# Kernel optimization log

Measured on AMD Instinct MI355X. Metric: run time of the kernel, lower is better.

Reference implementation:

```python
import jax, jax.numpy as jnp
import numpy as np

WS = 7        # window_size
NH = 12       # num_heads
HD = 32       # head_dim
SCALE = HD ** -0.5


def _rel_pos_index(ws: int) -> np.ndarray:
    # Static [N, N] index into the (2ws-1)^2 relative position bias table.
    coords = np.stack(np.meshgrid(np.arange(ws), np.arange(ws), indexing='ij'))
    coords = coords.reshape(2, -1)                       # [2, N]
    rel = coords[:, :, None] - coords[:, None, :]        # [2, N, N]
    rel = rel.transpose(1, 2, 0).copy()                  # [N, N, 2]
    rel[:, :, 0] += ws - 1
    rel[:, :, 1] += ws - 1
    rel[:, :, 0] *= 2 * ws - 1
    return rel.sum(-1)                                   # [N, N]

_REL_IDX = jnp.asarray(_rel_pos_index(WS))


def setup_inputs() -> dict:
    key = jax.random.key(0)
    ks = jax.random.split(key, 7)
    BW, N, C = 2048, WS * WS, 384
    nW = 64
    return {
        'x': jax.random.normal(ks[0], (BW, N, C), jnp.float32),
        'mask': jax.random.normal(ks[1], (nW, N, N), jnp.float32),
        'qkv_w': jax.random.normal(ks[2], (3 * C, C), jnp.float32) * 0.02,
        'qkv_b': jax.random.normal(ks[3], (3 * C,), jnp.float32) * 0.02,
        'proj_w': jax.random.normal(ks[4], (C, C), jnp.float32) * 0.02,
        'proj_b': jax.random.normal(ks[5], (C,), jnp.float32) * 0.02,
        'bias_table': jax.random.normal(ks[6], ((2 * WS - 1) ** 2, NH), jnp.float32) * 0.02,
    }


def reference(x, mask, qkv_w, qkv_b, proj_w, proj_b, bias_table):
    BW, N, C = x.shape
    # qkv projection: [BW, N, 3, H, hd]
    qkv = (x @ qkv_w.T + qkv_b).reshape(BW, N, 3, NH, HD)
    qkv = jnp.transpose(qkv, (2, 0, 3, 1, 4))            # [3, BW, H, N, hd]
    q, k, v = qkv[0], qkv[1], qkv[2]
    attn = jnp.einsum('bhnd,bhmd->bhnm', q, k) * SCALE   # [BW, H, N, N]
    # gathered relative position bias: [N, N, H] -> [H, N, N]
    bias = bias_table[_REL_IDX]                          # [N, N, H]
    attn = attn + jnp.transpose(bias, (2, 0, 1))[None]
    # shifted-window mask add: [nW, N, N] broadcast over batch and heads
    nW = mask.shape[0]
    attn = attn.reshape(BW // nW, nW, NH, N, N) + mask[None, :, None]
    attn = attn.reshape(BW, NH, N, N)
    attn = jax.nn.softmax(attn, axis=-1)
    out = jnp.einsum('bhnm,bhmd->bhnd', attn, v)         # [BW, H, N, hd]
    out = jnp.transpose(out, (0, 2, 1, 3)).reshape(BW, N, C)
    return out @ proj_w.T + proj_b
```

## Files before the change

### kernel.cpp

```cpp
#include <hip/hip_runtime.h>

typedef __attribute__((ext_vector_type(4))) float f32x4;
typedef __attribute__((ext_vector_type(8))) short s16x8;

#define MFMA16(a, b, c) __builtin_amdgcn_mfma_f32_16x16x32_bf16(a, b, c, 0, 0, 0)

static __device__ __forceinline__ unsigned short f2b(float f) {
  unsigned int u = __float_as_uint(f);
  u += 0x7fff + ((u >> 16) & 1);
  return (unsigned short)(u >> 16);
}

static __device__ __forceinline__ void gload_lds16(const unsigned short* g, unsigned short* l) {
  __builtin_amdgcn_global_load_lds(
      (const __attribute__((address_space(1))) unsigned int*)g,
      (__attribute__((address_space(3))) unsigned int*)l, 16, 0, 0);
}

#define BW    2048
#define NTOK  49
#define CDIM  384
#define NHEAD 12
#define HDIM  32
#define NWIN  64
#define MROWS (BW * NTOK)
#define SCALE 0.17677669529663687f
#define QK_ELEMS ((size_t)BW * NHEAD * NTOK * HDIM)

#define OFF_X    ((size_t)0)
#define OFF_Q    ((size_t)77070336)
#define OFF_K    ((size_t)154140672)
#define OFF_QW   ((size_t)231211008)
#define OFF_PW   ((size_t)232095744)
#define OFF_COMB ((size_t)232390656)

__global__ __launch_bounds__(256) void cast_kernel(const float* __restrict__ src,
                                                   unsigned short* __restrict__ dst, int n4) {
  int i = blockIdx.x * 256 + threadIdx.x;
  if (i >= n4) return;
  float4 f = ((const float4*)src)[i];
  ushort4 o;
  o.x = f2b(f.x); o.y = f2b(f.y); o.z = f2b(f.z); o.w = f2b(f.w);
  ((ushort4*)dst)[i] = o;
}

__global__ __launch_bounds__(256) void build_comb(const float* __restrict__ mask,
                                                  const float* __restrict__ bias_table,
                                                  float* __restrict__ comb) {
  int idx = blockIdx.x * 256 + threadIdx.x;
  if (idx >= NWIN * NHEAD * NTOK * NTOK) return;
  int ij = idx % (NTOK * NTOK);
  int wh = idx / (NTOK * NTOK);
  int h = wh % NHEAD;
  int w = wh / NHEAD;
  int i = ij / NTOK, j = ij % NTOK;
  int yi = i / 7, xi = i % 7, yj = j / 7, xj = j % 7;
  int rel = (yi - yj + 6) * 13 + (xi - xj + 6);
  comb[idx] = mask[w * (NTOK * NTOK) + ij] + bias_table[rel * NHEAD + h];
}

template <int MODE>
__global__ __launch_bounds__(256) void gemm_bt(const unsigned short* __restrict__ A,
                                               const unsigned short* __restrict__ Bt,
                                               const float* __restrict__ bias,
                                               void* __restrict__ Cv,
                                               unsigned short* __restrict__ vtb,
                                               int M, int N, int K) {
  __shared__ __align__(16) unsigned short As[128 * 32];
  __shared__ __align__(16) unsigned short Bs[128 * 32];
  const int tid = threadIdx.x;
  const int lane = tid & 63;
  const int wave = tid >> 6;
  const int lr = lane & 15, lg = lane >> 4;
  const int wm = (wave >> 1) * 64, wn = (wave & 1) * 64;
  const size_t tileM = (size_t)blockIdx.y * 128;
  const size_t tileN = (size_t)blockIdx.x * 128;

  const unsigned short* Ab = A + tileM * K;
  const unsigned short* Bb = Bt + tileN * K;

  const int c0 = tid, c1 = tid + 256;
  const size_t a0 = (size_t)(c0 >> 2) * K + (c0 & 3) * 8;
  const size_t a1 = (size_t)(c1 >> 2) * K + (c1 & 3) * 8;

  f32x4 acc[4][4] = {};

  for (int k0 = 0; k0 < K; k0 += 32) {
    gload_lds16(Ab + a0 + k0, As + c0 * 8);
    gload_lds16(Ab + a1 + k0, As + c1 * 8);
    gload_lds16(Bb + a0 + k0, Bs + c0 * 8);
    gload_lds16(Bb + a1 + k0, Bs + c1 * 8);
    __syncthreads();
    s16x8 af[4], bf[4];
#pragma unroll
    for (int mt = 0; mt < 4; ++mt)
      af[mt] = *(const s16x8*)&As[(wm + mt * 16 + lr) * 32 + lg * 8];
#pragma unroll
    for (int nt = 0; nt < 4; ++nt)
      bf[nt] = *(const s16x8*)&Bs[(wn + nt * 16 + lr) * 32 + lg * 8];
#pragma unroll
    for (int mt = 0; mt < 4; ++mt)
#pragma unroll
      for (int nt = 0; nt < 4; ++nt)
        acc[mt][nt] = MFMA16(af[mt], bf[nt], acc[mt][nt]);
    __syncthreads();
  }

  if (MODE == 0) {
    float* Cf = (float*)Cv;
#pragma unroll
    for (int nt = 0; nt < 4; ++nt) {
      const size_t gcol = tileN + wn + nt * 16 + lr;
      const float bv = bias[gcol];
#pragma unroll
      for (int mt = 0; mt < 4; ++mt)
#pragma unroll
        for (int r = 0; r < 4; ++r) {
          const size_t grow = tileM + wm + mt * 16 + lg * 4 + r;
          Cf[grow * (size_t)N + gcol] = acc[mt][nt][r] + bv;
        }
    }
  } else {
    unsigned short* qko = (unsigned short*)Cv;
    const int which = blockIdx.x / 3;
#pragma unroll
    for (int mt = 0; mt < 4; ++mt)
#pragma unroll
      for (int r = 0; r < 4; ++r) {
        const int grow = (int)tileM + wm + mt * 16 + lg * 4 + r;
        const int b = grow / 49;
        const int t = grow - b * 49;
#pragma unroll
        for (int nt = 0; nt < 4; ++nt) {
          const int gcol = (int)tileN + wn + nt * 16 + lr;
          const int cc = gcol - which * 384;
          const int hh = cc >> 5, d = cc & 31;
          const float v = acc[mt][nt][r] + bias[gcol];
          const size_t bh = (size_t)b * NHEAD + hh;
          if (which == 2) vtb[(bh * HDIM + d) * 64 + t] = f2b(v);
          else            qko[(size_t)which * QK_ELEMS + (bh * NTOK + t) * HDIM + d] = f2b(v);
        }
      }
  }
}

#define PSTR 72
__global__ __launch_bounds__(64) void attn_kernel(const unsigned short* __restrict__ q,
                                                  const unsigned short* __restrict__ k,
                                                  const unsigned short* __restrict__ vt,
                                                  const float* __restrict__ comb,
                                                  unsigned short* __restrict__ out) {
  __shared__ __align__(16) unsigned short Pt[64 * PSTR];
  const int b = blockIdx.x;
  const int h = blockIdx.y;
  const int lane = threadIdx.x;
  const int lr = lane & 15, lg = lane >> 4;
  const size_t bh = (size_t)b * NHEAD + h;
  const unsigned short* qb = q + bh * (NTOK * HDIM);
  const unsigned short* kb = k + bh * (NTOK * HDIM);
  const unsigned short* vb = vt + bh * (HDIM * 64);

  s16x8 qf[4], kf[4];
#pragma unroll
  for (int mt = 0; mt < 4; ++mt) {
    const int off = (mt * 16 + lr) * HDIM + lg * 8;
    qf[mt] = *(const s16x8*)(qb + off);
    kf[mt] = *(const s16x8*)(kb + off);
  }

  f32x4 S[4][4] = {};
#pragma unroll
  for (int mt = 0; mt < 4; ++mt)
#pragma unroll
    for (int nt = 0; nt < 4; ++nt)
      S[mt][nt] = MFMA16(qf[mt], kf[nt], S[mt][nt]);

  const float* cb = comb + ((size_t)(b & 63) * NHEAD + h) * (NTOK * NTOK);

#pragma unroll
  for (int mt = 0; mt < 4; ++mt) {
#pragma unroll
    for (int r = 0; r < 4; ++r) {
      const int row = mt * 16 + lg * 4 + r;
      const bool rowok = row < NTOK;
      float sv[4];
      float mx = -1e30f;
#pragma unroll
      for (int nt = 0; nt < 4; ++nt) {
        const int col = nt * 16 + lr;
        float s;
        if (col < NTOK)
          s = rowok ? S[mt][nt][r] * SCALE + cb[row * NTOK + col] : 0.0f;
        else
          s = -1e30f;
        sv[nt] = s;
        mx = fmaxf(mx, s);
      }
#pragma unroll
      for (int off = 8; off; off >>= 1) mx = fmaxf(mx, __shfl_xor(mx, off, 16));
      float sum = 0.f;
#pragma unroll
      for (int nt = 0; nt < 4; ++nt) {
        float e = exp2f((sv[nt] - mx) * 1.4426950408889634f);
        sv[nt] = e;
        sum += e;
      }
#pragma unroll
      for (int off = 8; off; off >>= 1) sum += __shfl_xor(sum, off, 16);
      const float inv = 1.0f / sum;
#pragma unroll
      for (int nt = 0; nt < 4; ++nt)
        Pt[row * PSTR + nt * 16 + lr] = f2b(sv[nt] * inv);
    }
  }
  __syncthreads();

  f32x4 O[4][2] = {};
#pragma unroll
  for (int ks = 0; ks < 2; ++ks) {
    s16x8 pf[4], vf[2];
#pragma unroll
    for (int mt = 0; mt < 4; ++mt)
      pf[mt] = *(const s16x8*)&Pt[(mt * 16 + lr) * PSTR + ks * 32 + lg * 8];
#pragma unroll
    for (int n2 = 0; n2 < 2; ++n2)
      vf[n2] = *(const s16x8*)(vb + (n2 * 16 + lr) * 64 + ks * 32 + lg * 8);
#pragma unroll
    for (int mt = 0; mt < 4; ++mt)
#pragma unroll
      for (int n2 = 0; n2 < 2; ++n2)
        O[mt][n2] = MFMA16(pf[mt], vf[n2], O[mt][n2]);
  }

  unsigned short* ob = out + (size_t)b * NTOK * CDIM + h * HDIM;
#pragma unroll
  for (int mt = 0; mt < 4; ++mt)
#pragma unroll
    for (int r = 0; r < 4; ++r) {
      const int row = mt * 16 + lg * 4 + r;
      if (row < NTOK) {
#pragma unroll
        for (int n2 = 0; n2 < 2; ++n2)
          ob[(size_t)row * CDIM + n2 * 16 + lr] = f2b(O[mt][n2][r]);
      }
    }
}

extern "C" void kernel_launch(void* const* d_in, const int* in_sizes, int n_in,
                              void* d_out, int out_size, void* d_ws, size_t ws_size,
                              hipStream_t stream) {
  const float* x          = (const float*)d_in[0];
  const float* mask       = (const float*)d_in[1];
  const float* qkv_w      = (const float*)d_in[2];
  const float* qkv_b      = (const float*)d_in[3];
  const float* proj_w     = (const float*)d_in[4];
  const float* proj_b     = (const float*)d_in[5];
  const float* bias_table = (const float*)d_in[6];
  float* out = (float*)d_out;
  char* ws = (char*)d_ws;

  unsigned short* xb   = (unsigned short*)(ws + OFF_X);
  unsigned short* qb   = (unsigned short*)(ws + OFF_Q);
  unsigned short* kb   = (unsigned short*)(ws + OFF_K);
  unsigned short* qw   = (unsigned short*)(ws + OFF_QW);
  unsigned short* pw   = (unsigned short*)(ws + OFF_PW);
  float* comb          = (float*)(ws + OFF_COMB);
  unsigned short* vtb  = (unsigned short*)d_out;

  cast_kernel<<<(MROWS * CDIM / 4 + 255) / 256, 256, 0, stream>>>(x, xb, MROWS * CDIM / 4);
  cast_kernel<<<(3 * CDIM * CDIM / 4 + 255) / 256, 256, 0, stream>>>(qkv_w, qw, 3 * CDIM * CDIM / 4);
  cast_kernel<<<(CDIM * CDIM / 4 + 255) / 256, 256, 0, stream>>>(proj_w, pw, CDIM * CDIM / 4);

  {
    int n = NWIN * NHEAD * NTOK * NTOK;
    build_comb<<<(n + 255) / 256, 256, 0, stream>>>(mask, bias_table, comb);
  }

  gemm_bt<2><<<dim3((3 * CDIM) / 128, MROWS / 128), 256, 0, stream>>>(
      xb, qw, qkv_b, qb, vtb, MROWS, 3 * CDIM, CDIM);

  attn_kernel<<<dim3(BW, NHEAD), 64, 0, stream>>>(qb, kb, vtb, comb, xb);

  gemm_bt<0><<<dim3(CDIM / 128, MROWS / 128), 256, 0, stream>>>(
      xb, pw, proj_b, out, nullptr, MROWS, CDIM, CDIM);
}
```

Measured before the change: 764.5 us.

## Pad tokens to 64 and stage QKV epilogue through LDS for vector stores

Pads each 49-token window to 64 rows so the QKV GEMM tiles line up with windows. The epilogue writes results into LDS and then issues 16-byte vectorized stores for Q/K and a transposed V, replacing scattered 2-byte stores with per-element division. The block index is also linearized, M-fastest, so tiles sharing a weight column run together. The cost is about 30% more GEMM rows and cast traffic spent on zero padding, plus larger workspace buffers.

```diff
diff --git a/kernel.cpp b/kernel.cpp
--- a/kernel.cpp
+++ b/kernel.cpp
@@ -19,20 +19,42 @@
 
 #define BW    2048
 #define NTOK  49
+#define TPAD  64
 #define CDIM  384
 #define NHEAD 12
 #define HDIM  32
 #define NWIN  64
 #define MROWS (BW * NTOK)
+#define MPAD  (BW * TPAD)
 #define SCALE 0.17677669529663687f
-#define QK_ELEMS ((size_t)BW * NHEAD * NTOK * HDIM)
-
-#define OFF_X    ((size_t)0)
-#define OFF_Q    ((size_t)77070336)
-#define OFF_K    ((size_t)154140672)
-#define OFF_QW   ((size_t)231211008)
-#define OFF_PW   ((size_t)232095744)
-#define OFF_COMB ((size_t)232390656)
+#define QKP   ((size_t)BW * NHEAD * TPAD * HDIM)
+
+#define OFF_XP   ((size_t)0)
+#define OFF_Q    ((size_t)100663296)
+#define OFF_K    ((size_t)201326592)
+#define OFF_QW   ((size_t)301989888)
+#define OFF_PW   ((size_t)302874624)
+#define OFF_COMB ((size_t)303169536)
+
+__global__ __launch_bounds__(256) void cast_pad(const float* __restrict__ x,
+                                                unsigned short* __restrict__ xp) {
+  const int i = blockIdx.x * 256 + threadIdx.x;
+  const int prow = i / 48;
+  const int cc = i - prow * 48;
+  const int t = prow & 63;
+  s16x8 o;
+  if (t < NTOK) {
+    const int srow = (prow >> 6) * NTOK + t;
+    const float4* s = (const float4*)(x + (size_t)srow * CDIM + cc * 8);
+    float4 f0 = s[0], f1 = s[1];
+    o[0] = f2b(f0.x); o[1] = f2b(f0.y); o[2] = f2b(f0.z); o[3] = f2b(f0.w);
+    o[4] = f2b(f1.x); o[5] = f2b(f1.y); o[6] = f2b(f1.z); o[7] = f2b(f1.w);
+  } else {
+#pragma unroll
+    for (int j = 0; j < 8; ++j) o[j] = 0;
+  }
+  *(s16x8*)(xp + (size_t)prow * CDIM + cc * 8) = o;
+}
 
 __global__ __launch_bounds__(256) void cast_kernel(const float* __restrict__ src,
                                                    unsigned short* __restrict__ dst, int n4) {
@@ -59,22 +81,27 @@
   comb[idx] = mask[w * (NTOK * NTOK) + ij] + bias_table[rel * NHEAD + h];
 }
 
-template <int MODE>
+#define CSTR 136
+template <int MODE, int MT>
 __global__ __launch_bounds__(256) void gemm_bt(const unsigned short* __restrict__ A,
                                                const unsigned short* __restrict__ Bt,
                                                const float* __restrict__ bias,
                                                void* __restrict__ Cv,
                                                unsigned short* __restrict__ vtb,
-                                               int M, int N, int K) {
-  __shared__ __align__(16) unsigned short As[128 * 32];
-  __shared__ __align__(16) unsigned short Bs[128 * 32];
+                                               int N, int K) {
+  __shared__ __align__(16) unsigned short smem[MODE == 2 ? 128 * CSTR : 8192];
+  unsigned short* As = smem;
+  unsigned short* Bs = smem + 4096;
   const int tid = threadIdx.x;
   const int lane = tid & 63;
   const int wave = tid >> 6;
   const int lr = lane & 15, lg = lane >> 4;
   const int wm = (wave >> 1) * 64, wn = (wave & 1) * 64;
-  const size_t tileM = (size_t)blockIdx.y * 128;
-  const size_t tileN = (size_t)blockIdx.x * 128;
+  const int lin = blockIdx.x;
+  const int tm = lin % MT;
+  const int tn = lin / MT;
+  const size_t tileM = (size_t)tm * 128;
+  const size_t tileN = (size_t)tn * 128;
 
   const unsigned short* Ab = A + tileM * K;
   const unsigned short* Bb = Bt + tileN * K;
@@ -121,26 +148,48 @@
         }
     }
   } else {
-    unsigned short* qko = (unsigned short*)Cv;
-    const int which = blockIdx.x / 3;
+    float bv[4];
+#pragma unroll
+    for (int nt = 0; nt < 4; ++nt) bv[nt] = bias[tileN + wn + nt * 16 + lr];
 #pragma unroll
     for (int mt = 0; mt < 4; ++mt)
 #pragma unroll
       for (int r = 0; r < 4; ++r) {
-        const int grow = (int)tileM + wm + mt * 16 + lg * 4 + r;
-        const int b = grow / 49;
-        const int t = grow - b * 49;
-#pragma unroll
-        for (int nt = 0; nt < 4; ++nt) {
-          const int gcol = (int)tileN + wn + nt * 16 + lr;
-          const int cc = gcol - which * 384;
-          const int hh = cc >> 5, d = cc & 31;
-          const float v = acc[mt][nt][r] + bias[gcol];
-          const size_t bh = (size_t)b * NHEAD + hh;
-          if (which == 2) vtb[(bh * HDIM + d) * 64 + t] = f2b(v);
-          else            qko[(size_t)which * QK_ELEMS + (bh * NTOK + t) * HDIM + d] = f2b(v);
-        }
-      }
+        const int row = wm + mt * 16 + lg * 4 + r;
+#pragma unroll
+        for (int nt = 0; nt < 4; ++nt)
+          smem[row * CSTR + wn + nt * 16 + lr] = f2b(acc[mt][nt][r] + bv[nt]);
+      }
+    __syncthreads();
+
+    const int which = tn / 3;
+    if (which < 2) {
+      unsigned short* qko = (unsigned short*)Cv + (size_t)which * QKP;
+#pragma unroll
+      for (int i = 0; i < 8; ++i) {
+        const int c = i * 256 + tid;
+        const int row = c >> 4, cg = c & 15;
+        s16x8 v = *(const s16x8*)&smem[row * CSTR + cg * 8];
+        const int grow = (int)tileM + row;
+        const int b = grow >> 6, t = grow & 63;
+        const int col = (int)tileN + cg * 8 - which * CDIM;
+        const int hh = col >> 5, d0 = col & 31;
+        *(s16x8*)(qko + (((size_t)b * NHEAD + hh) * TPAD + t) * HDIM + d0) = v;
+      }
+    } else {
+#pragma unroll
+      for (int i = 0; i < 8; ++i) {
+        const int c = i * 256 + tid;
+        const int col = c >> 4, w = (c >> 3) & 1, tc = c & 7;
+        s16x8 v;
+#pragma unroll
+        for (int j = 0; j < 8; ++j) v[j] = smem[(w * 64 + tc * 8 + j) * CSTR + col];
+        const int b = tm * 2 + w;
+        const int cc = (int)tileN + col - 2 * CDIM;
+        const int hh = cc >> 5, d = cc & 31;
+        *(s16x8*)(vtb + (((size_t)b * NHEAD + hh) * HDIM + d) * TPAD + tc * 8) = v;
+      }
+    }
   }
 }
 
@@ -156,9 +205,9 @@
   const int lane = threadIdx.x;
   const int lr = lane & 15, lg = lane >> 4;
   const size_t bh = (size_t)b * NHEAD + h;
-  const unsigned short* qb = q + bh * (NTOK * HDIM);
-  const unsigned short* kb = k + bh * (NTOK * HDIM);
-  const unsigned short* vb = vt + bh * (HDIM * 64);
+  const unsigned short* qb = q + bh * (TPAD * HDIM);
+  const unsigned short* kb = k + bh * (TPAD * HDIM);
+  const unsigned short* vb = vt + bh * (HDIM * TPAD);
 
   s16x8 qf[4], kf[4];
 #pragma unroll
@@ -224,7 +273,7 @@
       pf[mt] = *(const s16x8*)&Pt[(mt * 16 + lr) * PSTR + ks * 32 + lg * 8];
 #pragma unroll
     for (int n2 = 0; n2 < 2; ++n2)
-      vf[n2] = *(const s16x8*)(vb + (n2 * 16 + lr) * 64 + ks * 32 + lg * 8);
+      vf[n2] = *(const s16x8*)(vb + (n2 * 16 + lr) * TPAD + ks * 32 + lg * 8);
 #pragma unroll
     for (int mt = 0; mt < 4; ++mt)
 #pragma unroll
@@ -259,7 +308,7 @@
   float* out = (float*)d_out;
   char* ws = (char*)d_ws;
 
-  unsigned short* xb   = (unsigned short*)(ws + OFF_X);
+  unsigned short* xp   = (unsigned short*)(ws + OFF_XP);
   unsigned short* qb   = (unsigned short*)(ws + OFF_Q);
   unsigned short* kb   = (unsigned short*)(ws + OFF_K);
   unsigned short* qw   = (unsigned short*)(ws + OFF_QW);
@@ -267,7 +316,7 @@
   float* comb          = (float*)(ws + OFF_COMB);
   unsigned short* vtb  = (unsigned short*)d_out;
 
-  cast_kernel<<<(MROWS * CDIM / 4 + 255) / 256, 256, 0, stream>>>(x, xb, MROWS * CDIM / 4);
+  cast_pad<<<(MPAD * 48) / 256, 256, 0, stream>>>(x, xp);
   cast_kernel<<<(3 * CDIM * CDIM / 4 + 255) / 256, 256, 0, stream>>>(qkv_w, qw, 3 * CDIM * CDIM / 4);
   cast_kernel<<<(CDIM * CDIM / 4 + 255) / 256, 256, 0, stream>>>(proj_w, pw, CDIM * CDIM / 4);
 
@@ -276,11 +325,11 @@
     build_comb<<<(n + 255) / 256, 256, 0, stream>>>(mask, bias_table, comb);
   }
 
-  gemm_bt<2><<<dim3((3 * CDIM) / 128, MROWS / 128), 256, 0, stream>>>(
-      xb, qw, qkv_b, qb, vtb, MROWS, 3 * CDIM, CDIM);
-
-  attn_kernel<<<dim3(BW, NHEAD), 64, 0, stream>>>(qb, kb, vtb, comb, xb);
-
-  gemm_bt<0><<<dim3(CDIM / 128, MROWS / 128), 256, 0, stream>>>(
-      xb, pw, proj_b, out, nullptr, MROWS, CDIM, CDIM);
-}
+  gemm_bt<2, MPAD / 128><<<(MPAD / 128) * (3 * CDIM / 128), 256, 0, stream>>>(
+      xp, qw, qkv_b, qb, vtb, 3 * CDIM, CDIM);
+
+  attn_kernel<<<dim3(BW, NHEAD), 64, 0, stream>>>(qb, kb, vtb, comb, xp);
+
+  gemm_bt<0, MROWS / 128><<<(MROWS / 128) * (CDIM / 128), 256, 0, stream>>>(
+      xp, pw, proj_b, out, nullptr, CDIM, CDIM);
+}
```

Measured after the change: 758.6 us. About the same (-0.8%).
